# Performance work log

Hardware: AMD Instinct MI355X
Metric: run time of the kernel (lower is better)

## Reference

```python
import jax, jax.numpy as jnp
import numpy as np

DIL = 1  # dilation (== padding for 3x3 stride-1)
KK = 9   # 3x3 kernel points


def setup_inputs() -> dict:
    key = jax.random.key(0)
    k1, k2, k3, k4 = jax.random.split(key, 4)
    B, C, H, W = 8, 64, 128, 128
    Cout = 64
    x = jax.random.normal(k1, (B, C, H, W), jnp.float32)
    # offset/mask conv: nn.Conv2d default init scale-ish; keep offsets moderate
    w_off = jax.random.normal(k2, (27, C, 3, 3), jnp.float32) * 0.02
    b_off = jax.random.uniform(k3, (27,), jnp.float32, -0.05, 0.05)
    # c2_msra_fill: std = sqrt(2 / (fan_in + fan_out)), fan_in = C*9
    std = float(np.sqrt(2.0 / (C * 9 + Cout)))
    w_dcn = jax.random.normal(k4, (Cout, C, 3, 3), jnp.float32) * std
    return {"x": x, "w_off": w_off, "b_off": b_off, "w_dcn": w_dcn}


def _conv3x3(x, w, b, dil):
    out = jax.lax.conv_general_dilated(
        x, w, window_strides=(1, 1), padding=[(dil, dil), (dil, dil)],
        rhs_dilation=(dil, dil), dimension_numbers=("NCHW", "OIHW", "NCHW"))
    return out + b[None, :, None, None]


def reference(x, w_off, b_off, w_dcn):
    B, C, H, W = x.shape
    Cout = w_dcn.shape[0]
    # offset/mask conv, chunk into offset_x / offset_y / mask, cat offsets
    om = _conv3x3(x, w_off, b_off, DIL)                  # [B,27,H,W]
    off_x, off_y, mask = jnp.split(om, 3, axis=1)        # each [B,9,H,W]
    offset = jnp.concatenate([off_x, off_y], axis=1)     # [B,18,H,W]
    mask = jax.nn.sigmoid(mask)                          # [B,9,H,W]
    # mmcv DCNv2 layout: offset channel 2k = dy_k, 2k+1 = dx_k
    off = offset.reshape(B, KK, 2, H, W)
    dy, dx = off[:, :, 0], off[:, :, 1]                  # [B,9,H,W]
    # base sampling grid: p = out_pos - pad + k*dil (stride 1, pad = dil)
    ky, kx = jnp.meshgrid(jnp.arange(3), jnp.arange(3), indexing="ij")
    ky = ky.reshape(KK).astype(jnp.float32)
    kx = kx.reshape(KK).astype(jnp.float32)
    base_y = (jnp.arange(H, dtype=jnp.float32)[None, :, None]
              - DIL + ky[:, None, None] * DIL)           # [9,H,1]
    base_x = (jnp.arange(W, dtype=jnp.float32)[None, None, :]
              - DIL + kx[:, None, None] * DIL)           # [9,1,W]
    py = dy + base_y[None]                               # [B,9,H,W]
    px = dx + base_x[None]
    # bilinear sample with zero padding outside the image
    y0 = jnp.floor(py)
    x0 = jnp.floor(px)
    xf = x.reshape(B, C, H * W)
    sampled = jnp.zeros((B, C, KK, H, W), x.dtype)
    for oy in (0.0, 1.0):
        for ox in (0.0, 1.0):
            yi = y0 + oy
            xi = x0 + ox
            wgt = (1.0 - jnp.abs(py - yi)) * (1.0 - jnp.abs(px - xi))
            valid = (yi >= 0) & (yi < H) & (xi >= 0) & (xi < W)
            yc = jnp.clip(yi, 0, H - 1).astype(jnp.int32)
            xc = jnp.clip(xi, 0, W - 1).astype(jnp.int32)
            idx = (yc * W + xc).reshape(B, KK * H * W)
            vals = jax.vmap(lambda f, i: jnp.take(f, i, axis=1))(xf, idx)
            vals = vals.reshape(B, C, KK, H, W)
            sampled = sampled + vals * (wgt * valid)[:, None]
    sampled = sampled * mask[:, None]                    # modulation
    # weighted reduction == conv with gathered patches
    out = jnp.einsum("bckhw,ock->bohw", sampled, w_dcn.reshape(Cout, C, KK))
    return out
```

## Files before the change

### kernel.cpp

```cpp
#include <hip/hip_runtime.h>
#include <math.h>

#define B_  8
#define C_  64
#define H_  128
#define W_  128
#define KK_ 9
#define CO_ 64
#define HW_ (H_*W_)
#define CK_ 576

typedef _Float16 f16x8 __attribute__((ext_vector_type(8)));
typedef _Float16 h2    __attribute__((ext_vector_type(2)));
typedef __attribute__((ext_vector_type(4))) float f32x4;

__device__ inline unsigned pkrtz(float a, float b){
    auto v = __builtin_amdgcn_cvt_pkrtz(a, b);
    union{decltype(v) h; unsigned u;} c; c.h = v; return c.u;
}
__device__ inline h2 u2h(unsigned u){ union{unsigned x; h2 h;} c; c.x = u; return c.h; }
__device__ inline unsigned h2u(h2 v){ union{h2 h; unsigned u;} c; c.h = v; return c.u; }
__device__ inline unsigned short f2h(float f){
    _Float16 h = (_Float16)f;
    union{_Float16 h; unsigned short s;} c; c.h = h; return c.s;
}
__device__ inline h2 bcast_lo(unsigned u){ return u2h(__builtin_amdgcn_perm(u, u, 0x01000100)); }
__device__ inline h2 bcast_hi(unsigned u){ return u2h(__builtin_amdgcn_perm(u, u, 0x03020302)); }

__global__ __launch_bounds__(256) void prep_all(
    const float* __restrict__ w_dcn, const float* __restrict__ w_off,
    unsigned short* __restrict__ w_bf, unsigned short* __restrict__ wA)
{
    int i = blockIdx.x * 256 + threadIdx.x;
    if (i < 64 * CK_) {
        int o = i / CK_, r = i % CK_;
        int tap = r >> 6, c = r & 63;
        w_bf[i] = f2h(w_dcn[o * CK_ + c * 9 + tap]);
    } else {
        int j = i - 64 * CK_;
        int o = j / CK_, r = j % CK_;
        int tap = r >> 6, c = r & 63;
        float v = (o < 27) ? w_off[o * CK_ + c * 9 + tap] : 0.f;
        wA[j] = f2h(v);
    }
}

__global__ __launch_bounds__(256) void transpose3(const float* __restrict__ x,
                                                  unsigned short* __restrict__ xt)
{
    __shared__ unsigned tb[64 * 33];
    int b = blockIdx.x >> 8;
    int pixbase = (blockIdx.x & 255) * 64;
    int t = threadIdx.x;
    #pragma unroll
    for (int i = 0; i < 8; ++i) {
        int idx = i * 256 + t;
        int cp = idx >> 6, pix = idx & 63;
        float f0 = x[((size_t)(b * C_) + 2 * cp    ) * HW_ + pixbase + pix];
        float f1 = x[((size_t)(b * C_) + 2 * cp + 1) * HW_ + pixbase + pix];
        tb[pix * 33 + cp] = pkrtz(f0, f1);
    }
    __syncthreads();
    unsigned* xo = (unsigned*)xt + ((size_t)b * HW_ + pixbase) * 32;
    #pragma unroll
    for (int i = 0; i < 2; ++i) {
        int idx = i * 256 + t;
        int pix = idx >> 3, j = idx & 7;
        uint4 v;
        v.x = tb[pix * 33 + j * 4 + 0];
        v.y = tb[pix * 33 + j * 4 + 1];
        v.z = tb[pix * 33 + j * 4 + 2];
        v.w = tb[pix * 33 + j * 4 + 3];
        *(uint4*)(xo + pix * 32 + j * 4) = v;
    }
}

#define SSTR4 400
__global__ __launch_bounds__(256, 5) void dcn8(
    const unsigned short* __restrict__ xt,
    const unsigned short* __restrict__ wA,
    const float* __restrict__ b_off,
    const unsigned short* __restrict__ w_bf,
    float* __restrict__ out)
{
    __shared__ __align__(16) unsigned char sS[64 * SSTR4];
    __shared__ uint2 scr_w[576];
    __shared__ int   scr_o[576];
    float* om = (float*)sS;

    int tile = blockIdx.x;
    int b  = tile >> 8;
    int p0 = (tile & 255) * 64;
    int y  = p0 >> 7;
    int x0 = p0 & 127;
    int t  = threadIdx.x;
    int lane = t & 63, w = t >> 6;
    int m = lane & 15, q = lane >> 4;

    const unsigned short* xbr = xt + (size_t)(b * HW_) * 64;

    {
        int o0c = (w & 1) * 16;
        int pxh = (w >> 1) * 32;

        f32x4 accc[2] = {};
        #pragma unroll
        for (int ky = 0; ky < 3; ++ky) {
            int yy = y + ky - 1;
            if (yy >= 0 && yy < H_) {
                const unsigned short* xr = xbr + (size_t)yy * W_ * 64;
                #pragma unroll
                for (int kx = 0; kx < 3; ++kx) {
                    int s2 = (ky * 3 + kx) * 2;
                    f16x8 A0 = *(const f16x8*)(wA + (o0c + m) * CK_ + s2 * 32 + q * 8);
                    f16x8 A1 = *(const f16x8*)(wA + (o0c + m) * CK_ + (s2 + 1) * 32 + q * 8);
                    #pragma unroll
                    for (int nt = 0; nt < 2; ++nt) {
                        int xbase = x0 + pxh + nt * 16;
                        int px = xbase + m + kx - 1;
                        f16x8 b0, b1;
                        bool ledge = (xbase == 0   && kx == 0);
                        bool redge = (xbase == 112 && kx == 2);
                        if (ledge || redge) {
                            int pc = min(max(px, 0), W_ - 1);
                            const unsigned short* p = xr + pc * 64 + q * 8;
                            b0 = *(const f16x8*)p;
                            b1 = *(const f16x8*)(p + 32);
                            if (px != pc) {
                                b0 = (f16x8){0,0,0,0,0,0,0,0};
                                b1 = (f16x8){0,0,0,0,0,0,0,0};
                            }
                        } else {
                            const unsigned short* p = xr + px * 64 + q * 8;
                            b0 = *(const f16x8*)p;
                            b1 = *(const f16x8*)(p + 32);
                        }
                        accc[nt] = __builtin_amdgcn_mfma_f32_16x16x32_f16(A0, b0, accc[nt], 0, 0, 0);
                        accc[nt] = __builtin_amdgcn_mfma_f32_16x16x32_f16(A1, b1, accc[nt], 0, 0, 0);
                    }
                }
            }
        }
        #pragma unroll
        for (int nt = 0; nt < 2; ++nt) {
            #pragma unroll
            for (int r = 0; r < 4; ++r) {
                int j = o0c + q * 4 + r;
                if (j < 27)
                    om[j * 65 + pxh + nt * 16 + m] = accc[nt][r] + b_off[j];
            }
        }
    }
    __syncthreads();

    for (int i = t; i < 576; i += 256) {
        int k = i >> 6, sp = i & 63;
        float dy = om[(2 * k)     * 65 + sp];
        float dx = om[(2 * k + 1) * 65 + sp];
        float mk = 1.f / (1.f + __expf(-om[(18 + k) * 65 + sp]));
        float py = dy + (float)(y - 1 + k / 3);
        float px = dx + (float)(x0 + sp - 1 + k % 3);
        float fy = floorf(py), fx = floorf(px);
        int iy = (int)fy, ix = (int)fx;
        float ay = py - fy, ax = px - fx;
        float wy0 = (iy >= 0  && iy < H_)     ? (1.f - ay) : 0.f;
        float wy1 = (iy >= -1 && iy < H_ - 1) ? ay         : 0.f;
        float wx0 = (ix >= 0  && ix < W_)     ? (1.f - ax) : 0.f;
        float wx1 = (ix >= -1 && ix < W_ - 1) ? ax         : 0.f;
        int iy0 = min(max(iy, 0), H_ - 1);
        int iy1 = min(max(iy + 1, 0), H_ - 1);
        int ix0 = min(max(ix, 0), W_ - 1);
        int ix1 = min(max(ix + 1, 0), W_ - 1);
        float w00 = wy0*wx0*mk, w01 = wy0*wx1*mk, w10 = wy1*wx0*mk, w11 = wy1*wx1*mk;
        uint2 wv;
        wv.x = pkrtz(w00, w01);
        wv.y = pkrtz(w10, w11);
        scr_w[i] = wv;
        int off00 = (iy0 * W_ + ix0) * 128;
        scr_o[i] = off00 | ((ix1 != ix0) << 22) | ((iy1 != iy0) << 23);
    }

    int o0 = w * 16;
    __syncthreads();

    int cq = lane & 7;
    int g  = lane >> 3;
    const unsigned char* xb = (const unsigned char*)xbr;
    f32x4 acc[4] = {};
    int piB = w * 8 + g;

    uint2 wA_, wB_; int pB_;
    uint4 a00, a01, a10, a11;
    {
        wA_ = scr_w[piB];      int oo = scr_o[piB];
        wB_ = scr_w[piB + 32]; pB_ = scr_o[piB + 32];
        const unsigned char* a0 = xb + (oo & 0x3FFFFF) + cq * 16;
        int dxb = (oo >> 15) & 128;
        int dyb = (oo >> 9)  & 16384;
        a00 = *(const uint4*)(a0);
        a01 = *(const uint4*)(a0 + dxb);
        a10 = *(const uint4*)(a0 + dyb);
        a11 = *(const uint4*)(a0 + dyb + dxb);
    }

    #pragma unroll
    for (int chunk = 0; chunk < 3; ++chunk) {
        #pragma unroll
        for (int it6 = 0; it6 < 6; ++it6) {
            int k = chunk * 6 + it6;
            uint2 wC_ = {}; int pC_ = 0;
            if (k + 2 < 18) {
                int P = piB + (k + 2) * 32;
                wC_ = scr_w[P]; pC_ = scr_o[P];
            }
            uint4 n00 = {}, n01 = {}, n10 = {}, n11 = {};
            if (k + 1 < 18) {
                const unsigned char* a0 = xb + (pB_ & 0x3FFFFF) + cq * 16;
                int dxb = (pB_ >> 15) & 128;
                int dyb = (pB_ >> 9)  & 16384;
                n00 = *(const uint4*)(a0);
                n01 = *(const uint4*)(a0 + dxb);
                n10 = *(const uint4*)(a0 + dyb);
                n11 = *(const uint4*)(a0 + dyb + dxb);
            }
            h2 w00 = bcast_lo(wA_.x), w01 = bcast_hi(wA_.x);
            h2 w10 = bcast_lo(wA_.y), w11 = bcast_hi(wA_.y);
            uint4 o4;
            h2 r;
            r = w00*u2h(a00.x) + w01*u2h(a01.x) + w10*u2h(a10.x) + w11*u2h(a11.x); o4.x = h2u(r);
            r = w00*u2h(a00.y) + w01*u2h(a01.y) + w10*u2h(a10.y) + w11*u2h(a11.y); o4.y = h2u(r);
            r = w00*u2h(a00.z) + w01*u2h(a01.z) + w10*u2h(a10.z) + w11*u2h(a11.z); o4.z = h2u(r);
            r = w00*u2h(a00.w) + w01*u2h(a01.w) + w10*u2h(a10.w) + w11*u2h(a11.w); o4.w = h2u(r);
            int P = piB + k * 32;
            int sp = P & 63;
            int ktl = (P >> 6) - chunk * 3;
            *(uint4*)&sS[sp * SSTR4 + ktl * 128 + cq * 16] = o4;
            wA_ = wB_; wB_ = wC_; pB_ = pC_;
            a00 = n00; a01 = n01; a10 = n10; a11 = n11;
        }
        f16x8 Af[6];
        #pragma unroll
        for (int s = 0; s < 6; ++s)
            Af[s] = *(const f16x8*)(w_bf + (o0 + m) * CK_ + (chunk * 6 + s) * 32 + q * 8);
        __syncthreads();

        #pragma unroll
        for (int s = 0; s < 6; ++s) {
            #pragma unroll
            for (int nt = 0; nt < 4; ++nt) {
                f16x8 bb = *(const f16x8*)&sS[(nt * 16 + m) * SSTR4 + s * 64 + q * 16];
                acc[nt] = __builtin_amdgcn_mfma_f32_16x16x32_f16(Af[s], bb, acc[nt], 0, 0, 0);
            }
        }
        __syncthreads();
    }

    #pragma unroll
    for (int nt = 0; nt < 4; ++nt) {
        #pragma unroll
        for (int r = 0; r < 4; ++r) {
            int o = o0 + q * 4 + r;
            out[((size_t)(b * CO_ + o)) * HW_ + p0 + nt * 16 + m] = acc[nt][r];
        }
    }
}

extern "C" void kernel_launch(void* const* d_in, const int* in_sizes, int n_in,
                              void* d_out, int out_size, void* d_ws, size_t ws_size,
                              hipStream_t stream)
{
    const float* x     = (const float*)d_in[0];
    const float* w_off = (const float*)d_in[1];
    const float* b_off = (const float*)d_in[2];
    const float* w_dcn = (const float*)d_in[3];
    float* out = (float*)d_out;

    unsigned short* xt   = (unsigned short*)d_ws;
    unsigned short* w_bf = xt + (size_t)B_ * HW_ * 64;
    unsigned short* wA   = w_bf + 64 * CK_;

    prep_all<<<216, 256, 0, stream>>>(w_dcn, w_off, w_bf, wA);
    transpose3<<<B_ * 256, 256, 0, stream>>>(x, xt);
    dcn8<<<B_ * 256, 256, 0, stream>>>(xt, wA, b_off, w_bf, out);
}
```

Measured before the change: 176.2 us.

## Merge prep kernels, remap tile order, deepen gather prefetch, and lighten barriers

Folds the weight-prep kernel into the transpose kernel so one launch is saved. Remaps block index to tile so consecutive blocks span different batches, which changes the L2/cache locality pattern. Double-buffers the bilinear gather with two register sets and prefetches the scratch weights and offsets four steps ahead to hide more global-load latency. Replaces __syncthreads with a barrier that waits only on LDS counters, drops the final barrier, and raises wave priority around the MFMA loop. The extra prefetch registers may cut occupancy.

```diff
diff --git a/kernel.cpp b/kernel.cpp
--- a/kernel.cpp
+++ b/kernel.cpp
@@ -27,28 +27,29 @@
 __device__ inline h2 bcast_lo(unsigned u){ return u2h(__builtin_amdgcn_perm(u, u, 0x01000100)); }
 __device__ inline h2 bcast_hi(unsigned u){ return u2h(__builtin_amdgcn_perm(u, u, 0x03020302)); }
 
-__global__ __launch_bounds__(256) void prep_all(
+#define BAR_LGKM() asm volatile("s_waitcnt lgkmcnt(0)\n\ts_barrier" ::: "memory")
+
+__global__ __launch_bounds__(256) void transpose_prep(
+    const float* __restrict__ x, unsigned short* __restrict__ xt,
     const float* __restrict__ w_dcn, const float* __restrict__ w_off,
     unsigned short* __restrict__ w_bf, unsigned short* __restrict__ wA)
 {
-    int i = blockIdx.x * 256 + threadIdx.x;
-    if (i < 64 * CK_) {
-        int o = i / CK_, r = i % CK_;
-        int tap = r >> 6, c = r & 63;
-        w_bf[i] = f2h(w_dcn[o * CK_ + c * 9 + tap]);
-    } else {
-        int j = i - 64 * CK_;
-        int o = j / CK_, r = j % CK_;
-        int tap = r >> 6, c = r & 63;
-        float v = (o < 27) ? w_off[o * CK_ + c * 9 + tap] : 0.f;
-        wA[j] = f2h(v);
-    }
-}
-
-__global__ __launch_bounds__(256) void transpose3(const float* __restrict__ x,
-                                                  unsigned short* __restrict__ xt)
-{
     __shared__ unsigned tb[64 * 33];
+    if (blockIdx.x >= B_ * 256) {
+        int i = (blockIdx.x - B_ * 256) * 256 + threadIdx.x;
+        if (i < 64 * CK_) {
+            int o = i / CK_, r = i % CK_;
+            int tap = r >> 6, c = r & 63;
+            w_bf[i] = f2h(w_dcn[o * CK_ + c * 9 + tap]);
+        } else {
+            int j = i - 64 * CK_;
+            int o = j / CK_, r = j % CK_;
+            int tap = r >> 6, c = r & 63;
+            float v = (o < 27) ? w_off[o * CK_ + c * 9 + tap] : 0.f;
+            wA[j] = f2h(v);
+        }
+        return;
+    }
     int b = blockIdx.x >> 8;
     int pixbase = (blockIdx.x & 255) * 64;
     int t = threadIdx.x;
@@ -76,7 +77,7 @@
 }
 
 #define SSTR4 400
-__global__ __launch_bounds__(256, 5) void dcn8(
+__global__ __launch_bounds__(256, 5) void dcn9(
     const unsigned short* __restrict__ xt,
     const unsigned short* __restrict__ wA,
     const float* __restrict__ b_off,
@@ -88,7 +89,8 @@
     __shared__ int   scr_o[576];
     float* om = (float*)sS;
 
-    int tile = blockIdx.x;
+    int bid = blockIdx.x;
+    int tile = (bid & 7) * 256 + (bid >> 3);
     int b  = tile >> 8;
     int p0 = (tile & 255) * 64;
     int y  = p0 >> 7;
@@ -189,61 +191,73 @@
     f32x4 acc[4] = {};
     int piB = w * 8 + g;
 
-    uint2 wA_, wB_; int pB_;
-    uint4 a00, a01, a10, a11;
+#define GATHER(SET, OFF) do {                                              \
+        const unsigned char* a0_ = xb + ((OFF) & 0x3FFFFF) + cq * 16;      \
+        int dxb_ = ((OFF) >> 15) & 128;                                    \
+        int dyb_ = ((OFF) >> 9)  & 16384;                                  \
+        SET[0] = *(const uint4*)(a0_);                                     \
+        SET[1] = *(const uint4*)(a0_ + dxb_);                              \
+        SET[2] = *(const uint4*)(a0_ + dyb_);                              \
+        SET[3] = *(const uint4*)(a0_ + dyb_ + dxb_);                       \
+    } while (0)
+
+#define BLEND_STORE(SET, WQ, K) do {                                       \
+        h2 w00 = bcast_lo((WQ).x), w01 = bcast_hi((WQ).x);                 \
+        h2 w10 = bcast_lo((WQ).y), w11 = bcast_hi((WQ).y);                 \
+        uint4 o4; h2 r;                                                    \
+        r = w00*u2h(SET[0].x) + w01*u2h(SET[1].x)                          \
+          + w10*u2h(SET[2].x) + w11*u2h(SET[3].x); o4.x = h2u(r);          \
+        r = w00*u2h(SET[0].y) + w01*u2h(SET[1].y)                          \
+          + w10*u2h(SET[2].y) + w11*u2h(SET[3].y); o4.y = h2u(r);          \
+        r = w00*u2h(SET[0].z) + w01*u2h(SET[1].z)                          \
+          + w10*u2h(SET[2].z) + w11*u2h(SET[3].z); o4.z = h2u(r);          \
+        r = w00*u2h(SET[0].w) + w01*u2h(SET[1].w)                          \
+          + w10*u2h(SET[2].w) + w11*u2h(SET[3].w); o4.w = h2u(r);          \
+        *(uint4*)&sS[(piB + ((K)&1)*32) * SSTR4                            \
+                     + (((K)>>1) % 3) * 128 + cq * 16] = o4;               \
+    } while (0)
+
+    uint4 csA[4], csB[4];
+    uint2 sw0, sw1, sw2, sw3;
+    int so2, so3;
     {
-        wA_ = scr_w[piB];      int oo = scr_o[piB];
-        wB_ = scr_w[piB + 32]; pB_ = scr_o[piB + 32];
-        const unsigned char* a0 = xb + (oo & 0x3FFFFF) + cq * 16;
-        int dxb = (oo >> 15) & 128;
-        int dyb = (oo >> 9)  & 16384;
-        a00 = *(const uint4*)(a0);
-        a01 = *(const uint4*)(a0 + dxb);
-        a10 = *(const uint4*)(a0 + dyb);
-        a11 = *(const uint4*)(a0 + dyb + dxb);
+        sw0 = scr_w[piB];
+        sw1 = scr_w[piB + 32];
+        sw2 = scr_w[piB + 64];  so2 = scr_o[piB + 64];
+        sw3 = scr_w[piB + 96];  so3 = scr_o[piB + 96];
+        int oo0 = scr_o[piB];
+        int oo1 = scr_o[piB + 32];
+        GATHER(csA, oo0);
+        GATHER(csB, oo1);
     }
 
     #pragma unroll
     for (int chunk = 0; chunk < 3; ++chunk) {
         #pragma unroll
         for (int it6 = 0; it6 < 6; ++it6) {
-            int k = chunk * 6 + it6;
-            uint2 wC_ = {}; int pC_ = 0;
-            if (k + 2 < 18) {
-                int P = piB + (k + 2) * 32;
-                wC_ = scr_w[P]; pC_ = scr_o[P];
-            }
-            uint4 n00 = {}, n01 = {}, n10 = {}, n11 = {};
-            if (k + 1 < 18) {
-                const unsigned char* a0 = xb + (pB_ & 0x3FFFFF) + cq * 16;
-                int dxb = (pB_ >> 15) & 128;
-                int dyb = (pB_ >> 9)  & 16384;
-                n00 = *(const uint4*)(a0);
-                n01 = *(const uint4*)(a0 + dxb);
-                n10 = *(const uint4*)(a0 + dyb);
-                n11 = *(const uint4*)(a0 + dyb + dxb);
-            }
-            h2 w00 = bcast_lo(wA_.x), w01 = bcast_hi(wA_.x);
-            h2 w10 = bcast_lo(wA_.y), w11 = bcast_hi(wA_.y);
-            uint4 o4;
-            h2 r;
-            r = w00*u2h(a00.x) + w01*u2h(a01.x) + w10*u2h(a10.x) + w11*u2h(a11.x); o4.x = h2u(r);
-            r = w00*u2h(a00.y) + w01*u2h(a01.y) + w10*u2h(a10.y) + w11*u2h(a11.y); o4.y = h2u(r);
-            r = w00*u2h(a00.z) + w01*u2h(a01.z) + w10*u2h(a10.z) + w11*u2h(a11.z); o4.z = h2u(r);
-            r = w00*u2h(a00.w) + w01*u2h(a01.w) + w10*u2h(a10.w) + w11*u2h(a11.w); o4.w = h2u(r);
-            int P = piB + k * 32;
-            int sp = P & 63;
-            int ktl = (P >> 6) - chunk * 3;
-            *(uint4*)&sS[sp * SSTR4 + ktl * 128 + cq * 16] = o4;
-            wA_ = wB_; wB_ = wC_; pB_ = pC_;
-            a00 = n00; a01 = n01; a10 = n10; a11 = n11;
+            const int k = chunk * 6 + it6;
+            uint2 swN = {}; int soN = 0;
+            if (k + 4 < 18) {
+                int P = piB + (k + 4) * 32;
+                swN = scr_w[P]; soN = scr_o[P];
+            }
+            if (k & 1) {
+                BLEND_STORE(csB, sw0, k);
+                if (k + 2 < 18) GATHER(csB, so2);
+            } else {
+                BLEND_STORE(csA, sw0, k);
+                if (k + 2 < 18) GATHER(csA, so2);
+            }
+            sw0 = sw1; sw1 = sw2; sw2 = sw3; sw3 = swN;
+            so2 = so3; so3 = soN;
         }
         f16x8 Af[6];
         #pragma unroll
         for (int s = 0; s < 6; ++s)
             Af[s] = *(const f16x8*)(w_bf + (o0 + m) * CK_ + (chunk * 6 + s) * 32 + q * 8);
-        __syncthreads();
-
+        BAR_LGKM();
+
+        __builtin_amdgcn_s_setprio(1);
         #pragma unroll
         for (int s = 0; s < 6; ++s) {
             #pragma unroll
@@ -252,7 +266,8 @@
                 acc[nt] = __builtin_amdgcn_mfma_f32_16x16x32_f16(Af[s], bb, acc[nt], 0, 0, 0);
             }
         }
-        __syncthreads();
+        __builtin_amdgcn_s_setprio(0);
+        if (chunk < 2) BAR_LGKM();
     }
 
     #pragma unroll
@@ -263,6 +278,8 @@
             out[((size_t)(b * CO_ + o)) * HW_ + p0 + nt * 16 + m] = acc[nt][r];
         }
     }
+#undef GATHER
+#undef BLEND_STORE
 }
 
 extern "C" void kernel_launch(void* const* d_in, const int* in_sizes, int n_in,
@@ -279,7 +296,6 @@
     unsigned short* w_bf = xt + (size_t)B_ * HW_ * 64;
     unsigned short* wA   = w_bf + 64 * CK_;
 
-    prep_all<<<216, 256, 0, stream>>>(w_dcn, w_off, w_bf, wA);
-    transpose3<<<B_ * 256, 256, 0, stream>>>(x, xt);
-    dcn8<<<B_ * 256, 256, 0, stream>>>(xt, wA, b_off, w_bf, out);
-}
+    transpose_prep<<<B_ * 256 + 216, 256, 0, stream>>>(x, xt, w_dcn, w_off, w_bf, wA);
+    dcn9<<<B_ * 256, 256, 0, stream>>>(xt, wA, b_off, w_bf, out);
+}
```

Result: slower. 184.3 us (+4.6%).

## Merge prep into transpose launch, swizzle LDS tile, use lighter barriers and priority

Applied to the files above, without the earlier changes.

Folds the weight-prep kernel into the transpose kernel as extra blocks, which removes one launch. Shrinks the LDS row stride to 384 and applies an XOR swizzle to avoid bank conflicts on the sampled-tile writes and MFMA B-operand reads. Replaces __syncthreads with an inline-asm lgkmcnt wait plus s_barrier, skips the final barrier, and raises wave priority around the MFMA loop. The swizzle must match on both the write and read sides, and the reduced stride also shrinks LDS use.

```diff
diff --git a/kernel.cpp b/kernel.cpp
--- a/kernel.cpp
+++ b/kernel.cpp
@@ -27,28 +27,29 @@
 __device__ inline h2 bcast_lo(unsigned u){ return u2h(__builtin_amdgcn_perm(u, u, 0x01000100)); }
 __device__ inline h2 bcast_hi(unsigned u){ return u2h(__builtin_amdgcn_perm(u, u, 0x03020302)); }
 
-__global__ __launch_bounds__(256) void prep_all(
+#define BAR_LGKM() asm volatile("s_waitcnt lgkmcnt(0)\n\ts_barrier" ::: "memory")
+
+__global__ __launch_bounds__(256) void transpose_prep(
+    const float* __restrict__ x, unsigned short* __restrict__ xt,
     const float* __restrict__ w_dcn, const float* __restrict__ w_off,
     unsigned short* __restrict__ w_bf, unsigned short* __restrict__ wA)
 {
-    int i = blockIdx.x * 256 + threadIdx.x;
-    if (i < 64 * CK_) {
-        int o = i / CK_, r = i % CK_;
-        int tap = r >> 6, c = r & 63;
-        w_bf[i] = f2h(w_dcn[o * CK_ + c * 9 + tap]);
-    } else {
-        int j = i - 64 * CK_;
-        int o = j / CK_, r = j % CK_;
-        int tap = r >> 6, c = r & 63;
-        float v = (o < 27) ? w_off[o * CK_ + c * 9 + tap] : 0.f;
-        wA[j] = f2h(v);
-    }
-}
-
-__global__ __launch_bounds__(256) void transpose3(const float* __restrict__ x,
-                                                  unsigned short* __restrict__ xt)
-{
     __shared__ unsigned tb[64 * 33];
+    if (blockIdx.x >= B_ * 256) {
+        int i = (blockIdx.x - B_ * 256) * 256 + threadIdx.x;
+        if (i < 64 * CK_) {
+            int o = i / CK_, r = i % CK_;
+            int tap = r >> 6, c = r & 63;
+            w_bf[i] = f2h(w_dcn[o * CK_ + c * 9 + tap]);
+        } else {
+            int j = i - 64 * CK_;
+            int o = j / CK_, r = j % CK_;
+            int tap = r >> 6, c = r & 63;
+            float v = (o < 27) ? w_off[o * CK_ + c * 9 + tap] : 0.f;
+            wA[j] = f2h(v);
+        }
+        return;
+    }
     int b = blockIdx.x >> 8;
     int pixbase = (blockIdx.x & 255) * 64;
     int t = threadIdx.x;
@@ -75,8 +76,10 @@
     }
 }
 
-#define SSTR4 400
-__global__ __launch_bounds__(256, 5) void dcn8(
+#define SSTR4 384
+__device__ inline int swz(int row, int col){ return row * SSTR4 + (col ^ ((row & 7) << 4)); }
+
+__global__ __launch_bounds__(256, 5) void dcn10(
     const unsigned short* __restrict__ xt,
     const unsigned short* __restrict__ wA,
     const float* __restrict__ b_off,
@@ -207,7 +210,7 @@
     for (int chunk = 0; chunk < 3; ++chunk) {
         #pragma unroll
         for (int it6 = 0; it6 < 6; ++it6) {
-            int k = chunk * 6 + it6;
+            const int k = chunk * 6 + it6;
             uint2 wC_ = {}; int pC_ = 0;
             if (k + 2 < 18) {
                 int P = piB + (k + 2) * 32;
@@ -225,16 +228,14 @@
             }
             h2 w00 = bcast_lo(wA_.x), w01 = bcast_hi(wA_.x);
             h2 w10 = bcast_lo(wA_.y), w11 = bcast_hi(wA_.y);
-            uint4 o4;
-            h2 r;
+            uint4 o4; h2 r;
             r = w00*u2h(a00.x) + w01*u2h(a01.x) + w10*u2h(a10.x) + w11*u2h(a11.x); o4.x = h2u(r);
             r = w00*u2h(a00.y) + w01*u2h(a01.y) + w10*u2h(a10.y) + w11*u2h(a11.y); o4.y = h2u(r);
             r = w00*u2h(a00.z) + w01*u2h(a01.z) + w10*u2h(a10.z) + w11*u2h(a11.z); o4.z = h2u(r);
             r = w00*u2h(a00.w) + w01*u2h(a01.w) + w10*u2h(a10.w) + w11*u2h(a11.w); o4.w = h2u(r);
-            int P = piB + k * 32;
-            int sp = P & 63;
-            int ktl = (P >> 6) - chunk * 3;
-            *(uint4*)&sS[sp * SSTR4 + ktl * 128 + cq * 16] = o4;
+            int sp  = (piB + (k & 1) * 32) & 63;
+            int ktl = it6 >> 1;
+            *(uint4*)&sS[swz(sp, ktl * 128 + cq * 16)] = o4;
             wA_ = wB_; wB_ = wC_; pB_ = pC_;
             a00 = n00; a01 = n01; a10 = n10; a11 = n11;
         }
@@ -242,17 +243,19 @@
         #pragma unroll
         for (int s = 0; s < 6; ++s)
             Af[s] = *(const f16x8*)(w_bf + (o0 + m) * CK_ + (chunk * 6 + s) * 32 + q * 8);
-        __syncthreads();
-
+        BAR_LGKM();
+
+        __builtin_amdgcn_s_setprio(1);
         #pragma unroll
         for (int s = 0; s < 6; ++s) {
             #pragma unroll
             for (int nt = 0; nt < 4; ++nt) {
-                f16x8 bb = *(const f16x8*)&sS[(nt * 16 + m) * SSTR4 + s * 64 + q * 16];
+                f16x8 bb = *(const f16x8*)&sS[swz(nt * 16 + m, s * 64 + q * 16)];
                 acc[nt] = __builtin_amdgcn_mfma_f32_16x16x32_f16(Af[s], bb, acc[nt], 0, 0, 0);
             }
         }
-        __syncthreads();
+        __builtin_amdgcn_s_setprio(0);
+        if (chunk < 2) BAR_LGKM();
     }
 
     #pragma unroll
@@ -279,7 +282,6 @@
     unsigned short* w_bf = xt + (size_t)B_ * HW_ * 64;
     unsigned short* wA   = w_bf + 64 * CK_;
 
-    prep_all<<<216, 256, 0, stream>>>(w_dcn, w_off, w_bf, wA);
-    transpose3<<<B_ * 256, 256, 0, stream>>>(x, xt);
-    dcn8<<<B_ * 256, 256, 0, stream>>>(xt, wA, b_off, w_bf, out);
-}
+    transpose_prep<<<B_ * 256 + 216, 256, 0, stream>>>(x, xt, w_dcn, w_off, w_bf, wA);
+    dcn10<<<B_ * 256, 256, 0, stream>>>(xt, wA, b_off, w_bf, out);
+}
```

Measured after the change: 181.7 us. +3.1%, slower.
